# Kernel optimization log

Hardware: AMD Instinct MI355X
Metric: run time of the kernel (lower is better)

The kernel has to match this reference:

```python
import jax, jax.numpy as jnp
import numpy as np

B, H, S, D, KG = 1, 8, 1024, 64, 10

def setup_inputs() -> dict:
    key = jax.random.key(0)
    ks = jax.random.split(key, 16)
    n = jax.random.normal
    u = jax.random.uniform
    return {
        'Q': n(ks[0], (B, H, S, D), dtype=jnp.float32),
        'K': n(ks[1], (B, H, S, D), dtype=jnp.float32),
        'V': n(ks[2], (B, H, S, D), dtype=jnp.float32),
        'distance_matrix': u(ks[3], (B, H, S, S), dtype=jnp.float32) * 10.0,
        'energy_matrix': u(ks[4], (B, H, S, S), dtype=jnp.float32) * 5.0,
        'mask': jnp.ones((B, H, S, S), dtype=jnp.int32),
        'mu_D': n(ks[5], (KG,), dtype=jnp.float32),
        'sigma_D': u(ks[6], (KG,), dtype=jnp.float32) + 0.5,  # keep sigma positive
        'b_D': n(ks[7], (KG,), dtype=jnp.float32) * 0.1,
        'mu_E': n(ks[8], (KG,), dtype=jnp.float32),
        'sigma_E': u(ks[9], (KG,), dtype=jnp.float32) + 0.5,
        'b_E': n(ks[10], (KG,), dtype=jnp.float32) * 0.1,
        'W1': n(ks[11], (KG, KG), dtype=jnp.float32) / np.sqrt(KG),
        'b1': jnp.zeros((KG,), dtype=jnp.float32),
        'W2': n(ks[12], (1, KG), dtype=jnp.float32) / np.sqrt(KG),
        'b2': jnp.zeros((1,), dtype=jnp.float32),
    }


def _rbf_mlp_bias(x, b, mu, sigma, W1, b1, W2, b2):
    # x: [B,H,S,S] -> Gaussian RBF features over K kernels, then small MLP -> [B,H,S,S]
    z = (x[..., None] + b - mu) / sigma                      # [B,H,S,S,K]
    inv_norm = 1.0 / (jnp.sqrt(2.0 * jnp.pi) * sigma)
    psi = jnp.exp(-0.5 * z * z) * inv_norm                   # [B,H,S,S,K]
    h = jax.nn.gelu(jnp.einsum('bhijk,lk->bhijl', psi, W1) + b1, approximate=False)
    return (jnp.einsum('bhijk,lk->bhijl', h, W2) + b2)[..., 0]


def reference(Q, K, V, distance_matrix, energy_matrix, mask,
              mu_D, sigma_D, b_D, mu_E, sigma_E, b_E, W1, b1, W2, b2):
    d_model = Q.shape[-1]
    scores = jnp.einsum('bhid,bhjd->bhij', Q, K) / np.sqrt(d_model * 2)
    scores = scores + _rbf_mlp_bias(distance_matrix, b_D, mu_D, sigma_D, W1, b1, W2, b2)
    scores = scores + _rbf_mlp_bias(energy_matrix, b_E, mu_E, sigma_E, W1, b1, W2, b2)
    scores = jnp.where(mask == 0, jnp.float32(-1e9), scores)
    attn = jax.nn.softmax(scores, axis=-1)
    return jnp.einsum('bhij,bhjd->bhid', attn, V)
```

## Files before the change

### kernel.cpp

```cpp
#include <hip/hip_runtime.h>
#include <math.h>

#define Hn 8
#define Sn 1024
#define Dn 64
#define KG 10

#define TN 2048
#define RD 10.25f
#define RE 5.125f

typedef __attribute__((ext_vector_type(8))) short bf16x8;
typedef __attribute__((ext_vector_type(4))) float f32x4;
typedef __attribute__((ext_vector_type(4))) _Float16 h16x4;
typedef unsigned short u16;
typedef unsigned int u32;

__device__ inline float bf2f(u16 u) {
    union { u32 i; float f; } v;
    v.i = ((u32)u) << 16;
    return v.f;
}

__device__ inline u16 f2bf(float f) {
    union { float f; u32 i; } v;
    v.f = f;
    u32 i = v.i;
    return (u16)((i + 0x7FFFu + ((i >> 16) & 1u)) >> 16);
}

__device__ inline u16 f2h_bits(float f) {
    union { _Float16 h; u16 u; } cv;
    cv.h = (_Float16)f;
    return cv.u;
}

__device__ float bias_eval(float x,
                           const float* __restrict__ mu, const float* __restrict__ sg,
                           const float* __restrict__ bb,
                           const float* __restrict__ W1, const float* __restrict__ b1,
                           const float* __restrict__ W2, const float* __restrict__ b2) {
    const float inv_s2pi = 0.39894228040143267794f;
    float psi[KG];
#pragma unroll
    for (int k = 0; k < KG; k++) {
        float s = sg[k];
        float z = (x + bb[k] - mu[k]) / s;
        psi[k] = __expf(-0.5f * z * z) * (inv_s2pi / s);
    }
    float out = b2[0];
#pragma unroll
    for (int l = 0; l < KG; l++) {
        float a = b1[l];
#pragma unroll
        for (int k = 0; k < KG; k++) a += psi[k] * W1[l * KG + k];
        float g = 0.5f * a * (1.0f + erff(a * 0.70710678118654752440f));
        out += g * W2[l];
    }
    return out;
}

__global__ __launch_bounds__(256) void build_tables_kernel(
    const float* __restrict__ muD, const float* __restrict__ sgD, const float* __restrict__ bD,
    const float* __restrict__ muE, const float* __restrict__ sgE, const float* __restrict__ bE,
    const float* __restrict__ W1, const float* __restrict__ b1,
    const float* __restrict__ W2, const float* __restrict__ b2,
    u32* __restrict__ tab)
{
    int id = blockIdx.x * 256 + threadIdx.x;
    int which = (id >= TN);
    int idx = id & (TN - 1);
    float h = (which ? RE : RD) / (float)TN;
    float x0 = idx * h;
    float v0, v1;
    if (which) {
        v0 = bias_eval(x0,     muE, sgE, bE, W1, b1, W2, b2);
        v1 = bias_eval(x0 + h, muE, sgE, bE, W1, b1, W2, b2);
    } else {
        v0 = bias_eval(x0,     muD, sgD, bD, W1, b1, W2, b2);
        v1 = bias_eval(x0 + h, muD, sgD, bD, W1, b1, W2, b2);
    }
    tab[id] = (u32)f2bf(v0) | ((u32)f2bf(v1 - v0) << 16);
}

__global__ __launch_bounds__(256) void prep_kernel(
    const float* __restrict__ Dm, const float* __restrict__ Em, const int* __restrict__ Mk,
    const float* __restrict__ Q, const float* __restrict__ K, const float* __restrict__ V,
    const u32* __restrict__ tab,
    u16* __restrict__ Bb, u16* __restrict__ Qb, u16* __restrict__ Kb, u16* __restrict__ VTi)
{
    __shared__ __align__(16) u32 sTab[2 * TN];
    const int wg = blockIdx.x;
    const int tid = threadIdx.x;

    if (wg < 4096) {
        {
            const uint4* g4 = (const uint4*)tab;
            uint4* s4 = (uint4*)sTab;
#pragma unroll
            for (int i = 0; i < 4; i++) s4[tid + 256 * i] = g4[tid + 256 * i];
        }
        __syncthreads();

        const float invhD = (float)TN / RD;
        const float invhE = (float)TN / RE;
        const size_t base = ((size_t)wg * 256 + tid) * 8;

        const float4 d0 = *(const float4*)(Dm + base);
        const float4 d1 = *(const float4*)(Dm + base + 4);
        const float4 e0 = *(const float4*)(Em + base);
        const float4 e1 = *(const float4*)(Em + base + 4);
        const int4   m0 = *(const int4*)(Mk + base);
        const int4   m1 = *(const int4*)(Mk + base + 4);

        const float dv[8] = {d0.x, d0.y, d0.z, d0.w, d1.x, d1.y, d1.z, d1.w};
        const float ev[8] = {e0.x, e0.y, e0.z, e0.w, e1.x, e1.y, e1.z, e1.w};
        const int   mv[8] = {m0.x, m0.y, m0.z, m0.w, m1.x, m1.y, m1.z, m1.w};

        u16 ob[8];
#pragma unroll
        for (int j = 0; j < 8; j++) {
            float tf = dv[j] * invhD;
            int i = min((int)tf, TN - 1);
            float fr = tf - (float)i;
            u32 p = sTab[i];
            float vD = fmaf(bf2f((u16)(p >> 16)), fr, bf2f((u16)p));

            tf = ev[j] * invhE;
            i = min((int)tf, TN - 1);
            fr = tf - (float)i;
            p = sTab[TN + i];
            float vE = fmaf(bf2f((u16)(p >> 16)), fr, bf2f((u16)p));

            float v = vD + vE;
            v = fminf(fmaxf(v, -60.f), 64.f);
            v = (mv[j] == 0) ? -60.f : v;
            ob[j] = f2h_bits(v);
        }
        *(uint4*)(Bb + base) = *(const uint4*)ob;
    } else if (wg < 5120) {
        int i = (wg - 4096) * 256 + tid;
        int arr = i >> 17;
        i &= (1 << 17) - 1;
        float4 v = ((const float4*)(arr ? K : Q))[i];
        ushort4 o;
        o.x = f2bf(v.x); o.y = f2bf(v.y); o.z = f2bf(v.z); o.w = f2bf(v.w);
        ((ushort4*)(arr ? Kb : Qb))[i] = o;
    } else {
        int g = (wg - 5120) * 256 + tid;
        int h = g >> 16;
        int d = (g >> 10) & 63;
        int s = g & 1023;
        int t = s >> 5, q = (s >> 3) & 3, j = s & 7;
        int src_s = (t << 5) + (q << 2) + (j & 3) + ((j >> 2) << 4);
        VTi[g] = f2bf(V[(((size_t)h << 10) + src_s) * Dn + d]);
    }
}

__global__ __launch_bounds__(256, 4) void attn_kernel(
    const u16* __restrict__ Qb, const u16* __restrict__ Kb, const u16* __restrict__ VTi,
    const u16* __restrict__ Bb, float* __restrict__ out)
{
    __shared__ float sO[4][16][68];
    __shared__ float sL[4][16];

    const int tid  = threadIdx.x;
    const int h    = blockIdx.y;
    const int q0   = blockIdx.x * 16;
    const int wave = tid >> 6;
    const int lane = tid & 63;
    const int quad = lane >> 4;
    const int l16  = lane & 15;

    const u16* Qh = Qb  + (size_t)h * Sn * Dn;
    const u16* Kh = Kb  + (size_t)h * Sn * Dn;
    const u16* Vh = VTi + (size_t)h * Dn * Sn;
    const u16* Bh = Bb  + ((size_t)(h * Sn + q0 + l16)) * Sn;
    const float scale = 0.08838834764831845f;

    const bf16x8 bQ0 = *(const bf16x8*)(Qh + (q0 + l16) * Dn + quad * 8);
    const bf16x8 bQ1 = *(const bf16x8*)(Qh + (q0 + l16) * Dn + 32 + quad * 8);

    f32x4 O0 = {0.f, 0.f, 0.f, 0.f}, O1 = O0, O2 = O0, O3 = O0;
    float l_r = 0.f;

    const int kbase = wave * 256;
    const u16* krb = Kh + (size_t)l16 * Dn + quad * 8;
    const u16* vrb = Vh + quad * 8;

    bf16x8 cK[2][4];
    h16x4  cB[2][2];

    {
        const u16* kr = krb + (size_t)kbase * Dn;
        cK[0][0] = *(const bf16x8*)(kr);
        cK[0][1] = *(const bf16x8*)(kr + 32);
        cK[0][2] = *(const bf16x8*)(kr + 16 * Dn);
        cK[0][3] = *(const bf16x8*)(kr + 16 * Dn + 32);
        cB[0][0] = *(const h16x4*)(Bh + kbase + quad * 4);
        cB[0][1] = *(const h16x4*)(Bh + kbase + 16 + quad * 4);
    }

#pragma unroll
    for (int t = 0; t < 8; t++) {
        const int cur = t & 1, nxt = cur ^ 1;
        const int k0 = kbase + t * 32;

        if (t < 7) {
            const int kn = k0 + 32;
            const u16* kr = krb + (size_t)kn * Dn;
            cK[nxt][0] = *(const bf16x8*)(kr);
            cK[nxt][1] = *(const bf16x8*)(kr + 32);
            cK[nxt][2] = *(const bf16x8*)(kr + 16 * Dn);
            cK[nxt][3] = *(const bf16x8*)(kr + 16 * Dn + 32);
            cB[nxt][0] = *(const h16x4*)(Bh + kn + quad * 4);
            cB[nxt][1] = *(const h16x4*)(Bh + kn + 16 + quad * 4);
        }

        const u16* vr = vrb + k0;
        const bf16x8 bV0 = *(const bf16x8*)(vr + (size_t)(l16)      * Sn);
        const bf16x8 bV1 = *(const bf16x8*)(vr + (size_t)(16 + l16) * Sn);
        const bf16x8 bV2 = *(const bf16x8*)(vr + (size_t)(32 + l16) * Sn);
        const bf16x8 bV3 = *(const bf16x8*)(vr + (size_t)(48 + l16) * Sn);

        f32x4 s0 = {0.f, 0.f, 0.f, 0.f}, s1 = s0;
        s0 = __builtin_amdgcn_mfma_f32_16x16x32_bf16(cK[cur][0], bQ0, s0, 0, 0, 0);
        s0 = __builtin_amdgcn_mfma_f32_16x16x32_bf16(cK[cur][1], bQ1, s0, 0, 0, 0);
        s1 = __builtin_amdgcn_mfma_f32_16x16x32_bf16(cK[cur][2], bQ0, s1, 0, 0, 0);
        s1 = __builtin_amdgcn_mfma_f32_16x16x32_bf16(cK[cur][3], bQ1, s1, 0, 0, 0);

        bf16x8 aP;
#pragma unroll
        for (int r = 0; r < 4; r++) {
            const float p0 = __expf(fmaf(s0[r], scale, (float)cB[cur][0][r]));
            const float p1 = __expf(fmaf(s1[r], scale, (float)cB[cur][1][r]));
            l_r += p0 + p1;
            aP[r]     = (short)f2bf(p0);
            aP[4 + r] = (short)f2bf(p1);
        }

        O0 = __builtin_amdgcn_mfma_f32_16x16x32_bf16(aP, bV0, O0, 0, 0, 0);
        O1 = __builtin_amdgcn_mfma_f32_16x16x32_bf16(aP, bV1, O1, 0, 0, 0);
        O2 = __builtin_amdgcn_mfma_f32_16x16x32_bf16(aP, bV2, O2, 0, 0, 0);
        O3 = __builtin_amdgcn_mfma_f32_16x16x32_bf16(aP, bV3, O3, 0, 0, 0);
    }

    l_r += __shfl_xor(l_r, 16, 64);
    l_r += __shfl_xor(l_r, 32, 64);
    if (lane < 16) sL[wave][lane] = l_r;

#pragma unroll
    for (int r = 0; r < 4; r++) {
        sO[wave][quad * 4 + r][ 0 + l16] = O0[r];
        sO[wave][quad * 4 + r][16 + l16] = O1[r];
        sO[wave][quad * 4 + r][32 + l16] = O2[r];
        sO[wave][quad * 4 + r][48 + l16] = O3[r];
    }
    __syncthreads();

    const int row = tid >> 4;
    const int c4  = (tid & 15) * 4;
    float lg = 0.f;
#pragma unroll
    for (int w = 0; w < 4; w++) lg += sL[w][row];
    const float inv = 1.0f / lg;

    float acc[4];
#pragma unroll
    for (int c = 0; c < 4; c++) {
        acc[c] = 0.f;
#pragma unroll
        for (int w = 0; w < 4; w++) acc[c] += sO[w][row][c4 + c];
        acc[c] *= inv;
    }
    float4 ov = {acc[0], acc[1], acc[2], acc[3]};
    *(float4*)(out + ((size_t)(h * Sn + q0 + row)) * Dn + c4) = ov;
}

extern "C" void kernel_launch(void* const* d_in, const int* in_sizes, int n_in,
                              void* d_out, int out_size, void* d_ws, size_t ws_size,
                              hipStream_t stream) {
    const float* Q    = (const float*)d_in[0];
    const float* K    = (const float*)d_in[1];
    const float* V    = (const float*)d_in[2];
    const float* Dm   = (const float*)d_in[3];
    const float* Em   = (const float*)d_in[4];
    const int*   Mask = (const int*)d_in[5];
    const float* muD  = (const float*)d_in[6];
    const float* sgD  = (const float*)d_in[7];
    const float* bD   = (const float*)d_in[8];
    const float* muE  = (const float*)d_in[9];
    const float* sgE  = (const float*)d_in[10];
    const float* bE   = (const float*)d_in[11];
    const float* W1   = (const float*)d_in[12];
    const float* b1   = (const float*)d_in[13];
    const float* W2   = (const float*)d_in[14];
    const float* b2   = (const float*)d_in[15];

    u32* tab = (u32*)d_ws;
    u16* Qb  = (u16*)((char*)d_ws + 2 * TN * 4);
    u16* Kb  = Qb + (size_t)Hn * Sn * Dn;
    u16* VTi = Kb + (size_t)Hn * Sn * Dn;
    u16* Bb  = VTi + (size_t)Hn * Sn * Dn;

    build_tables_kernel<<<2 * TN / 256, 256, 0, stream>>>(
        muD, sgD, bD, muE, sgE, bE, W1, b1, W2, b2, tab);

    prep_kernel<<<7168, 256, 0, stream>>>(Dm, Em, Mask, Q, K, V, tab,
                                          Bb, Qb, Kb, VTi);

    dim3 grid(Sn / 16, Hn);
    attn_kernel<<<grid, 256, 0, stream>>>(Qb, Kb, VTi, Bb, (float*)d_out);
}
```

Before: 186.7 us.

## Fuse bias table lookup into attention kernel and tile V transpose via LDS

Bias computation (table interpolation over distance/energy/mask) moves from the prep kernel into the attention kernel, so each block builds its 16x1024 fp16 bias rows in shared memory. This removes the write and re-read of the 16 MB fp16 bias buffer in global memory. The V transpose is also rewritten to stage 64x64 tiles in LDS, giving coalesced reads and writes in place of strided gathers. In exchange the attention kernel needs much more LDS (about 33 KB bias plus a 16 KB table/output union), which can lower occupancy, and it adds a serial prologue before the MFMA loop.

```diff
diff --git a/kernel.cpp b/kernel.cpp
--- a/kernel.cpp
+++ b/kernel.cpp
@@ -84,62 +84,14 @@
 }
 
 __global__ __launch_bounds__(256) void prep_kernel(
-    const float* __restrict__ Dm, const float* __restrict__ Em, const int* __restrict__ Mk,
     const float* __restrict__ Q, const float* __restrict__ K, const float* __restrict__ V,
-    const u32* __restrict__ tab,
-    u16* __restrict__ Bb, u16* __restrict__ Qb, u16* __restrict__ Kb, u16* __restrict__ VTi)
+    u16* __restrict__ Qb, u16* __restrict__ Kb, u16* __restrict__ VTi)
 {
-    __shared__ __align__(16) u32 sTab[2 * TN];
-    const int wg = blockIdx.x;
-    const int tid = threadIdx.x;
-
-    if (wg < 4096) {
-        {
-            const uint4* g4 = (const uint4*)tab;
-            uint4* s4 = (uint4*)sTab;
-#pragma unroll
-            for (int i = 0; i < 4; i++) s4[tid + 256 * i] = g4[tid + 256 * i];
-        }
-        __syncthreads();
-
-        const float invhD = (float)TN / RD;
-        const float invhE = (float)TN / RE;
-        const size_t base = ((size_t)wg * 256 + tid) * 8;
-
-        const float4 d0 = *(const float4*)(Dm + base);
-        const float4 d1 = *(const float4*)(Dm + base + 4);
-        const float4 e0 = *(const float4*)(Em + base);
-        const float4 e1 = *(const float4*)(Em + base + 4);
-        const int4   m0 = *(const int4*)(Mk + base);
-        const int4   m1 = *(const int4*)(Mk + base + 4);
-
-        const float dv[8] = {d0.x, d0.y, d0.z, d0.w, d1.x, d1.y, d1.z, d1.w};
-        const float ev[8] = {e0.x, e0.y, e0.z, e0.w, e1.x, e1.y, e1.z, e1.w};
-        const int   mv[8] = {m0.x, m0.y, m0.z, m0.w, m1.x, m1.y, m1.z, m1.w};
-
-        u16 ob[8];
-#pragma unroll
-        for (int j = 0; j < 8; j++) {
-            float tf = dv[j] * invhD;
-            int i = min((int)tf, TN - 1);
-            float fr = tf - (float)i;
-            u32 p = sTab[i];
-            float vD = fmaf(bf2f((u16)(p >> 16)), fr, bf2f((u16)p));
-
-            tf = ev[j] * invhE;
-            i = min((int)tf, TN - 1);
-            fr = tf - (float)i;
-            p = sTab[TN + i];
-            float vE = fmaf(bf2f((u16)(p >> 16)), fr, bf2f((u16)p));
-
-            float v = vD + vE;
-            v = fminf(fmaxf(v, -60.f), 64.f);
-            v = (mv[j] == 0) ? -60.f : v;
-            ob[j] = f2h_bits(v);
-        }
-        *(uint4*)(Bb + base) = *(const uint4*)ob;
-    } else if (wg < 5120) {
-        int i = (wg - 4096) * 256 + tid;
+    __shared__ float tile[64][68];
+    const int wg = blockIdx.x, tid = threadIdx.x;
+
+    if (wg < 1024) {
+        int i = wg * 256 + tid;
         int arr = i >> 17;
         i &= (1 << 17) - 1;
         float4 v = ((const float4*)(arr ? K : Q))[i];
@@ -147,26 +99,104 @@
         o.x = f2bf(v.x); o.y = f2bf(v.y); o.z = f2bf(v.z); o.w = f2bf(v.w);
         ((ushort4*)(arr ? Kb : Qb))[i] = o;
     } else {
-        int g = (wg - 5120) * 256 + tid;
-        int h = g >> 16;
-        int d = (g >> 10) & 63;
-        int s = g & 1023;
-        int t = s >> 5, q = (s >> 3) & 3, j = s & 7;
-        int src_s = (t << 5) + (q << 2) + (j & 3) + ((j >> 2) << 4);
-        VTi[g] = f2bf(V[(((size_t)h << 10) + src_s) * Dn + d]);
+        const int b  = wg - 1024;
+        const int h  = b >> 4;
+        const int s0 = (b & 15) * 64;
+        const int rr = tid >> 4, cc = (tid & 15) * 4;
+        const float* Vh = V + ((size_t)h * Sn + s0) * Dn;
+#pragma unroll
+        for (int i = 0; i < 4; i++) {
+            float4 v = *(const float4*)(Vh + (size_t)(i * 16 + rr) * Dn + cc);
+            tile[i * 16 + rr][cc]     = v.x;
+            tile[i * 16 + rr][cc + 1] = v.y;
+            tile[i * 16 + rr][cc + 2] = v.z;
+            tile[i * 16 + rr][cc + 3] = v.w;
+        }
+        __syncthreads();
+        u16* dst = VTi + (size_t)h * Dn * Sn + s0;
+#pragma unroll
+        for (int i = 0; i < 4; i++) {
+            const int d = i * 16 + rr;
+            u16 tmp[4];
+#pragma unroll
+            for (int j2 = 0; j2 < 4; j2++) {
+                int sp = cc + j2;
+                int q = (sp >> 3) & 3, j = sp & 7;
+                int s = (sp & ~31) + q * 4 + (j & 3) + ((j >> 2) << 4);
+                tmp[j2] = f2bf(tile[s][d]);
+            }
+            ushort4 o = {tmp[0], tmp[1], tmp[2], tmp[3]};
+            *(ushort4*)(dst + (size_t)d * Sn + cc) = o;
+        }
     }
 }
 
 __global__ __launch_bounds__(256, 4) void attn_kernel(
     const u16* __restrict__ Qb, const u16* __restrict__ Kb, const u16* __restrict__ VTi,
-    const u16* __restrict__ Bb, float* __restrict__ out)
+    const float* __restrict__ Dm, const float* __restrict__ Em, const int* __restrict__ Mk,
+    const u32* __restrict__ gtab, float* __restrict__ out)
 {
-    __shared__ float sO[4][16][68];
-    __shared__ float sL[4][16];
+    __shared__ u16 sBias[16][1032];
+    __shared__ union {
+        u32 tab[2 * TN];
+        struct { float O[4][16][68]; float L[4][16]; } f;
+    } sU;
 
     const int tid  = threadIdx.x;
     const int h    = blockIdx.y;
     const int q0   = blockIdx.x * 16;
+
+    {
+        const uint4* g4 = (const uint4*)gtab;
+        uint4* s4 = (uint4*)sU.tab;
+#pragma unroll
+        for (int i = 0; i < 4; i++) s4[tid + 256 * i] = g4[tid + 256 * i];
+    }
+    __syncthreads();
+
+    {
+        const float invhD = (float)TN / RD;
+        const float invhE = (float)TN / RE;
+        const int prow = tid >> 4;
+        const int pcb  = (tid & 15) * 4;
+        const size_t roff = ((size_t)h * Sn + q0 + prow) * Sn + pcb;
+        const float* Dr = Dm + roff;
+        const float* Er = Em + roff;
+        const int*   Mr = Mk + roff;
+
+#pragma unroll 4
+        for (int i = 0; i < 16; i++) {
+            const int c = pcb + i * 64;
+            const float4 d4 = *(const float4*)(Dr + i * 64);
+            const float4 e4 = *(const float4*)(Er + i * 64);
+            const int4   m4 = *(const int4*)(Mr + i * 64);
+            const float dv[4] = {d4.x, d4.y, d4.z, d4.w};
+            const float ev[4] = {e4.x, e4.y, e4.z, e4.w};
+            const int   mv[4] = {m4.x, m4.y, m4.z, m4.w};
+            u16 ob[4];
+#pragma unroll
+            for (int j = 0; j < 4; j++) {
+                float tf = dv[j] * invhD;
+                int ix = min((int)tf, TN - 1);
+                float fr = tf - (float)ix;
+                u32 p = sU.tab[ix];
+                float vD = fmaf(bf2f((u16)(p >> 16)), fr, bf2f((u16)p));
+
+                tf = ev[j] * invhE;
+                ix = min((int)tf, TN - 1);
+                fr = tf - (float)ix;
+                p = sU.tab[TN + ix];
+                float vE = fmaf(bf2f((u16)(p >> 16)), fr, bf2f((u16)p));
+
+                float v = fminf(fmaxf(vD + vE, -60.f), 64.f);
+                v = (mv[j] == 0) ? -60.f : v;
+                ob[j] = f2h_bits(v);
+            }
+            *(ushort4*)(&sBias[prow][c]) = *(const ushort4*)ob;
+        }
+    }
+    __syncthreads();
+
     const int wave = tid >> 6;
     const int lane = tid & 63;
     const int quad = lane >> 4;
@@ -175,7 +205,6 @@
     const u16* Qh = Qb  + (size_t)h * Sn * Dn;
     const u16* Kh = Kb  + (size_t)h * Sn * Dn;
     const u16* Vh = VTi + (size_t)h * Dn * Sn;
-    const u16* Bh = Bb  + ((size_t)(h * Sn + q0 + l16)) * Sn;
     const float scale = 0.08838834764831845f;
 
     const bf16x8 bQ0 = *(const bf16x8*)(Qh + (q0 + l16) * Dn + quad * 8);
@@ -189,16 +218,12 @@
     const u16* vrb = Vh + quad * 8;
 
     bf16x8 cK[2][4];
-    h16x4  cB[2][2];
-
     {
         const u16* kr = krb + (size_t)kbase * Dn;
         cK[0][0] = *(const bf16x8*)(kr);
         cK[0][1] = *(const bf16x8*)(kr + 32);
         cK[0][2] = *(const bf16x8*)(kr + 16 * Dn);
         cK[0][3] = *(const bf16x8*)(kr + 16 * Dn + 32);
-        cB[0][0] = *(const h16x4*)(Bh + kbase + quad * 4);
-        cB[0][1] = *(const h16x4*)(Bh + kbase + 16 + quad * 4);
     }
 
 #pragma unroll
@@ -207,14 +232,11 @@
         const int k0 = kbase + t * 32;
 
         if (t < 7) {
-            const int kn = k0 + 32;
-            const u16* kr = krb + (size_t)kn * Dn;
+            const u16* kr = krb + (size_t)(k0 + 32) * Dn;
             cK[nxt][0] = *(const bf16x8*)(kr);
             cK[nxt][1] = *(const bf16x8*)(kr + 32);
             cK[nxt][2] = *(const bf16x8*)(kr + 16 * Dn);
             cK[nxt][3] = *(const bf16x8*)(kr + 16 * Dn + 32);
-            cB[nxt][0] = *(const h16x4*)(Bh + kn + quad * 4);
-            cB[nxt][1] = *(const h16x4*)(Bh + kn + 16 + quad * 4);
         }
 
         const u16* vr = vrb + k0;
@@ -223,6 +245,9 @@
         const bf16x8 bV2 = *(const bf16x8*)(vr + (size_t)(32 + l16) * Sn);
         const bf16x8 bV3 = *(const bf16x8*)(vr + (size_t)(48 + l16) * Sn);
 
+        const h16x4 cb0 = *(const h16x4*)(&sBias[l16][k0 + quad * 4]);
+        const h16x4 cb1 = *(const h16x4*)(&sBias[l16][k0 + 16 + quad * 4]);
+
         f32x4 s0 = {0.f, 0.f, 0.f, 0.f}, s1 = s0;
         s0 = __builtin_amdgcn_mfma_f32_16x16x32_bf16(cK[cur][0], bQ0, s0, 0, 0, 0);
         s0 = __builtin_amdgcn_mfma_f32_16x16x32_bf16(cK[cur][1], bQ1, s0, 0, 0, 0);
@@ -232,8 +257,8 @@
         bf16x8 aP;
 #pragma unroll
         for (int r = 0; r < 4; r++) {
-            const float p0 = __expf(fmaf(s0[r], scale, (float)cB[cur][0][r]));
-            const float p1 = __expf(fmaf(s1[r], scale, (float)cB[cur][1][r]));
+            const float p0 = __expf(fmaf(s0[r], scale, (float)cb0[r]));
+            const float p1 = __expf(fmaf(s1[r], scale, (float)cb1[r]));
             l_r += p0 + p1;
             aP[r]     = (short)f2bf(p0);
             aP[4 + r] = (short)f2bf(p1);
@@ -247,14 +272,14 @@
 
     l_r += __shfl_xor(l_r, 16, 64);
     l_r += __shfl_xor(l_r, 32, 64);
-    if (lane < 16) sL[wave][lane] = l_r;
-
+    __syncthreads();
+    if (lane < 16) sU.f.L[wave][lane] = l_r;
 #pragma unroll
     for (int r = 0; r < 4; r++) {
-        sO[wave][quad * 4 + r][ 0 + l16] = O0[r];
-        sO[wave][quad * 4 + r][16 + l16] = O1[r];
-        sO[wave][quad * 4 + r][32 + l16] = O2[r];
-        sO[wave][quad * 4 + r][48 + l16] = O3[r];
+        sU.f.O[wave][quad * 4 + r][ 0 + l16] = O0[r];
+        sU.f.O[wave][quad * 4 + r][16 + l16] = O1[r];
+        sU.f.O[wave][quad * 4 + r][32 + l16] = O2[r];
+        sU.f.O[wave][quad * 4 + r][48 + l16] = O3[r];
     }
     __syncthreads();
 
@@ -262,7 +287,7 @@
     const int c4  = (tid & 15) * 4;
     float lg = 0.f;
 #pragma unroll
-    for (int w = 0; w < 4; w++) lg += sL[w][row];
+    for (int w = 0; w < 4; w++) lg += sU.f.L[w][row];
     const float inv = 1.0f / lg;
 
     float acc[4];
@@ -270,7 +295,7 @@
     for (int c = 0; c < 4; c++) {
         acc[c] = 0.f;
 #pragma unroll
-        for (int w = 0; w < 4; w++) acc[c] += sO[w][row][c4 + c];
+        for (int w = 0; w < 4; w++) acc[c] += sU.f.O[w][row][c4 + c];
         acc[c] *= inv;
     }
     float4 ov = {acc[0], acc[1], acc[2], acc[3]};
@@ -301,14 +326,13 @@
     u16* Qb  = (u16*)((char*)d_ws + 2 * TN * 4);
     u16* Kb  = Qb + (size_t)Hn * Sn * Dn;
     u16* VTi = Kb + (size_t)Hn * Sn * Dn;
-    u16* Bb  = VTi + (size_t)Hn * Sn * Dn;
 
     build_tables_kernel<<<2 * TN / 256, 256, 0, stream>>>(
         muD, sgD, bD, muE, sgE, bE, W1, b1, W2, b2, tab);
 
-    prep_kernel<<<7168, 256, 0, stream>>>(Dm, Em, Mask, Q, K, V, tab,
-                                          Bb, Qb, Kb, VTi);
+    prep_kernel<<<1152, 256, 0, stream>>>(Q, K, V, Qb, Kb, VTi);
 
     dim3 grid(Sn / 16, Hn);
-    attn_kernel<<<grid, 256, 0, stream>>>(Qb, Kb, VTi, Bb, (float*)d_out);
-}
+    attn_kernel<<<grid, 256, 0, stream>>>(Qb, Kb, VTi, Dm, Em, Mask, tab,
+                                          (float*)d_out);
+}
```

After: 179.2 us. -4.0%, faster.
